# Performance work log

Measured on AMD Instinct MI355X. Metric: run time of the kernel, lower is better.

Reference implementation:

```python
import jax, jax.numpy as jnp
import numpy as np

B, CH, S = 1024, 60, 288
F1, D, F2, NCLS, KL = 8, 2, 16, 4, 64
BN_EPS = 1e-3
PD_EPS = 1e-6  # torch.nn.PairwiseDistance default eps


def _conv(x, w, pad_w=0, groups=1):
    return jax.lax.conv_general_dilated(
        x, w, window_strides=(1, 1), padding=[(0, 0), (pad_w, pad_w)],
        dimension_numbers=("NCHW", "OIHW", "NCHW"), feature_group_count=groups)


def _bn(x, g, b, m, v):
    # eval-mode BatchNorm2d with running stats, eps=0.001
    inv = g / jnp.sqrt(v + BN_EPS)
    return x * inv[None, :, None, None] + (b - m * inv)[None, :, None, None]


def _avgpool_w(x, k):
    s = jax.lax.reduce_window(x, 0.0, jax.lax.add, (1, 1, 1, k), (1, 1, 1, k), "VALID")
    return s / k


def setup_inputs() -> dict:
    key = jax.random.key(0)
    ks = jax.random.split(key, 16)
    x = jax.random.normal(ks[0], (B, 1, CH, S), jnp.float32)
    y = jax.random.randint(ks[1], (B,), 0, NCLS, dtype=jnp.int32)
    conv1_w = jax.random.normal(ks[2], (F1, 1, 1, KL), jnp.float32) * 0.05
    dw = jax.random.normal(ks[3], (F1 * D, 1, CH, 1), jnp.float32) * 0.2
    # Conv2dWithConstraint: torch.renorm(w, p=2, dim=0, maxnorm=1) applied to .data
    norms = jnp.sqrt(jnp.sum(dw * dw, axis=(1, 2, 3), keepdims=True))
    dw_w = dw * jnp.minimum(1.0, 1.0 / jnp.maximum(norms, 1e-7))
    pw_w = jax.random.normal(ks[4], (F2, F1 * D, 1, 1), jnp.float32) * 0.1
    fc_w = jax.random.normal(ks[5], (NCLS, 144), jnp.float32) * 0.05
    fc_b = jnp.zeros((NCLS,), jnp.float32)

    def bnp(k, c):
        k1, k2, k3, k4 = jax.random.split(k, 4)
        g = 1.0 + 0.1 * jax.random.normal(k1, (c,), jnp.float32)
        b = 0.1 * jax.random.normal(k2, (c,), jnp.float32)
        m = 0.1 * jax.random.normal(k3, (c,), jnp.float32)
        v = jax.random.uniform(k4, (c,), jnp.float32, 0.5, 1.5)
        return g, b, m, v

    bn1_g, bn1_b, bn1_m, bn1_v = bnp(ks[6], F1)
    bn2_g, bn2_b, bn2_m, bn2_v = bnp(ks[7], F1 * D)
    bn3_g, bn3_b, bn3_m, bn3_v = bnp(ks[8], F2)
    return dict(x=x, y=y, conv1_w=conv1_w,
                bn1_g=bn1_g, bn1_b=bn1_b, bn1_m=bn1_m, bn1_v=bn1_v,
                dw_w=dw_w, bn2_g=bn2_g, bn2_b=bn2_b, bn2_m=bn2_m, bn2_v=bn2_v,
                pw_w=pw_w, bn3_g=bn3_g, bn3_b=bn3_b, bn3_m=bn3_m, bn3_v=bn3_v,
                fc_w=fc_w, fc_b=fc_b)


def _centroid_loss(feat, y):
    # per-class mean (torch code computes it from detached numpy -> stop_gradient)
    sums = jax.ops.segment_sum(feat, y, num_segments=NCLS)       # [NCLS, 144]
    cnts = jax.ops.segment_sum(jnp.ones((feat.shape[0],), feat.dtype), y, num_segments=NCLS)
    cent = jax.lax.stop_gradient(sums / jnp.maximum(cnts, 1.0)[:, None])
    diff = feat - cent[y] + PD_EPS                                # [B, 144]
    dist = jnp.sqrt(jnp.sum(diff * diff, axis=-1))                # [B]
    return jnp.mean(dist)


def reference(x, y, conv1_w, bn1_g, bn1_b, bn1_m, bn1_v,
              dw_w, bn2_g, bn2_b, bn2_m, bn2_v,
              pw_w, bn3_g, bn3_b, bn3_m, bn3_v, fc_w, fc_b):
    h = _conv(x, conv1_w, pad_w=KL // 2)                 # [B, F1, 60, 289]
    h = _bn(h, bn1_g, bn1_b, bn1_m, bn1_v)
    h = _conv(h, dw_w, pad_w=0, groups=F1)               # [B, F1*D, 1, 289]
    h = _bn(h, bn2_g, bn2_b, bn2_m, bn2_v)
    h = jax.nn.elu(h)
    h = _avgpool_w(h, 4)                                 # width 72 (dropout = eval no-op)
    h = _conv(h, pw_w)                                   # [B, F2, 1, 72]
    h = _bn(h, bn3_g, bn3_b, bn3_m, bn3_v)
    h = jax.nn.elu(h)
    h = _avgpool_w(h, 8)                                 # width 9
    feat = h.reshape(h.shape[0], -1)                     # [B, 144]
    cl = _centroid_loss(feat, y)
    probs = jax.nn.softmax(feat @ fc_w.T + fc_b, axis=1)
    return probs, cl
```

## Files before the change

### kernel.cpp

```cpp
#include <hip/hip_runtime.h>
#include <math.h>

#define NB   1024
#define CH   60
#define SW   288
#define F1C  8
#define FD   16
#define F2C  16
#define KLEN 64
#define NCLS 4
#define PWID 72
#define NV   9
#define FEAT 144
#define NTHR 320
#define ACH  30

#define XR_STRIDE 356
#define PH_STRIDE 76
#define W1_STRIDE 68

__device__ __forceinline__ float elu1(float v) {
    return v > 0.f ? v : __expf(v) - 1.f;
}

__device__ __forceinline__ unsigned short f2bf(float f) {
    unsigned int u = __float_as_uint(f);
    u = (u + 0x7fffu + ((u >> 16) & 1u)) >> 16;
    return (unsigned short)u;
}

__global__ __launch_bounds__(256, 8) void eegnet_chreduce(
    const float* __restrict__ x, const float* __restrict__ dw_w,
    unsigned short* __restrict__ xr,
    float* __restrict__ zero_ws,
    float* __restrict__ cl)
{
    __shared__ float s_part[2][FD][65];
    const int tid = threadIdx.x;
    if (blockIdx.x == 0) {
        for (int i = tid; i < 580; i += 256) zero_ws[i] = 0.f;
        if (tid == 0) cl[0] = 0.f;
    }
    const int wv   = tid >> 6;
    const int lane = tid & 63;
    const int h  = __builtin_amdgcn_readfirstlane(wv & 1);
    const int es = wv >> 1;
    const int e  = blockIdx.x * 2 + es;
    const int wflat = e * 64 + lane;
    const int b = wflat / SW;
    const int w = wflat - b * SW;

    const float* xp = x + (size_t)b * (CH * SW) + (size_t)(h * ACH) * SW + w;
    float v[ACH];
    #pragma unroll
    for (int j = 0; j < ACH; ++j) v[j] = xp[j * SW];

    float acc[FD];
    #pragma unroll
    for (int f = 0; f < FD; ++f) acc[f] = 0.f;
    #pragma unroll
    for (int j = 0; j < ACH; ++j) {
        const float xv = v[j];
        #pragma unroll
        for (int f = 0; f < FD; ++f)
            acc[f] = fmaf(dw_w[f * CH + h * ACH + j], xv, acc[f]);
    }

    if (h == 1) {
        #pragma unroll
        for (int f = 0; f < FD; ++f) s_part[es][f][lane] = acc[f];
    }
    __syncthreads();
    if (h == 0) {
        const size_t base = (size_t)b * (FD * SW) + w;
        #pragma unroll
        for (int f = 0; f < FD; ++f)
            xr[base + f * SW] = f2bf(acc[f] + s_part[es][f][lane]);
    }
}

__global__ __launch_bounds__(NTHR, 4) void eegnet_head(
    const unsigned int* __restrict__ xr, const int* __restrict__ y,
    const float* __restrict__ conv1_w,
    const float* __restrict__ bn1_g, const float* __restrict__ bn1_b,
    const float* __restrict__ bn1_m, const float* __restrict__ bn1_v,
    const float* __restrict__ dw_w,
    const float* __restrict__ bn2_g, const float* __restrict__ bn2_b,
    const float* __restrict__ bn2_m, const float* __restrict__ bn2_v,
    const float* __restrict__ pw_w,
    const float* __restrict__ bn3_g, const float* __restrict__ bn3_b,
    const float* __restrict__ bn3_m, const float* __restrict__ bn3_v,
    const float* __restrict__ fc_w, const float* __restrict__ fc_b,
    float* __restrict__ probs_out, float* __restrict__ feat_out,
    float* __restrict__ sums_out, int* __restrict__ cnt_out)
{
    __shared__ __align__(16) float s_xr[FD * XR_STRIDE];
    __shared__ __align__(16) float s_w1[F1C * W1_STRIDE];
    __shared__ __align__(16) float s_ph[FD * PH_STRIDE];
    __shared__ float s_pwT[FD * F2C];
    __shared__ float s_feat[FEAT];
    __shared__ float s_A[FD], s_Cb[FD], s_a3[F2C], s_c3[F2C];

    const int tid = threadIdx.x;
    const int b = blockIdx.x;

    if (tid == 0) atomicAdd(&cnt_out[y[b]], 1);
    for (int i = tid; i < F1C * KLEN; i += NTHR)
        s_w1[(i >> 6) * W1_STRIDE + (i & 63)] = conv1_w[i];
    for (int i = tid; i < F2C * FD; i += NTHR)
        s_pwT[(i & 15) * F2C + (i >> 4)] = pw_w[i];
    for (int i = tid; i < FD * 68; i += NTHR) {
        int f = i / 68, p = i % 68;
        int wp = (p < 32) ? p : (288 + p);
        s_xr[f * XR_STRIDE + wp] = 0.f;
    }
    {
        const uint4* xrb = (const uint4*)(xr + (size_t)b * (FD * 144));
        for (int i = tid; i < 576; i += NTHR) {
            const int f = i / 36;
            const int k = i - f * 36;
            const uint4 v = xrb[i];
            float* dst = &s_xr[f * XR_STRIDE + 32 + 8 * k];
            float4 lo, hi;
            lo.x = __uint_as_float(v.x << 16); lo.y = __uint_as_float(v.x & 0xffff0000u);
            lo.z = __uint_as_float(v.y << 16); lo.w = __uint_as_float(v.y & 0xffff0000u);
            hi.x = __uint_as_float(v.z << 16); hi.y = __uint_as_float(v.z & 0xffff0000u);
            hi.z = __uint_as_float(v.w << 16); hi.w = __uint_as_float(v.w & 0xffff0000u);
            *(float4*)dst = lo;
            *(float4*)(dst + 4) = hi;
        }
    }
    if (tid < FD) {
        const int f = tid, f1 = f >> 1;
        const float inv1 = bn1_g[f1] / sqrtf(bn1_v[f1] + 1e-3f);
        const float c1 = bn1_b[f1] - bn1_m[f1] * inv1;
        const float inv2 = bn2_g[f] / sqrtf(bn2_v[f] + 1e-3f);
        const float c2 = bn2_b[f] - bn2_m[f] * inv2;
        float sdw = 0.f;
        for (int ch = 0; ch < CH; ++ch) sdw += dw_w[f * CH + ch];
        s_A[f] = inv2 * inv1;
        s_Cb[f] = inv2 * c1 * sdw + c2;
        const float inv3 = bn3_g[f] / sqrtf(bn3_v[f] + 1e-3f);
        s_a3[f] = inv3;
        s_c3[f] = bn3_b[f] - bn3_m[f] * inv3;
    }
    __syncthreads();

    if (tid < 288) {
        const int f = tid & 15;
        const int q = tid >> 4;
        const float4* xp = (const float4*)&s_xr[f * XR_STRIDE + 16 * q];
        const float4* wp = (const float4*)&s_w1[(f >> 1) * W1_STRIDE];
        float cw[20];
        #pragma unroll
        for (int i = 0; i < 4; ++i) {
            const float4 t = xp[i];
            cw[4*i] = t.x; cw[4*i+1] = t.y; cw[4*i+2] = t.z; cw[4*i+3] = t.w;
        }
        float bb[16];
        #pragma unroll
        for (int j = 0; j < 16; ++j) bb[j] = 0.f;
        #pragma unroll
        for (int m = 0; m < 16; ++m) {
            {
                const float4 t = xp[m + 4];
                const int s = (4 * (m + 4)) % 20;
                cw[s] = t.x; cw[s+1] = t.y; cw[s+2] = t.z; cw[s+3] = t.w;
            }
            const float4 wv = wp[m];
            #pragma unroll
            for (int j = 0; j < 16; ++j) {
                bb[j] = fmaf(wv.x, cw[(4*m + j    ) % 20], bb[j]);
                bb[j] = fmaf(wv.y, cw[(4*m + j + 1) % 20], bb[j]);
                bb[j] = fmaf(wv.z, cw[(4*m + j + 2) % 20], bb[j]);
                bb[j] = fmaf(wv.w, cw[(4*m + j + 3) % 20], bb[j]);
            }
        }
        const float Af = s_A[f], Cf = s_Cb[f];
        float e[16];
        #pragma unroll
        for (int j = 0; j < 16; ++j) e[j] = elu1(fmaf(Af, bb[j], Cf));
        float4 ph;
        ph.x = (e[0]  + e[1]  + e[2]  + e[3])  * 0.25f;
        ph.y = (e[4]  + e[5]  + e[6]  + e[7])  * 0.25f;
        ph.z = (e[8]  + e[9]  + e[10] + e[11]) * 0.25f;
        ph.w = (e[12] + e[13] + e[14] + e[15]) * 0.25f;
        *(float4*)&s_ph[f * PH_STRIDE + 4 * q] = ph;
    }
    __syncthreads();

    if (tid < FEAT) {
        const int f2 = tid / NV;
        const int v = tid - f2 * NV;
        float su[8];
        #pragma unroll
        for (int k = 0; k < 8; ++k) su[k] = 0.f;
        #pragma unroll
        for (int f = 0; f < FD; ++f) {
            const float w = s_pwT[f * F2C + f2];
            const float4 p0 = *(const float4*)&s_ph[f * PH_STRIDE + 8 * v];
            const float4 p1 = *(const float4*)&s_ph[f * PH_STRIDE + 8 * v + 4];
            su[0] = fmaf(w, p0.x, su[0]); su[1] = fmaf(w, p0.y, su[1]);
            su[2] = fmaf(w, p0.z, su[2]); su[3] = fmaf(w, p0.w, su[3]);
            su[4] = fmaf(w, p1.x, su[4]); su[5] = fmaf(w, p1.y, su[5]);
            su[6] = fmaf(w, p1.z, su[6]); su[7] = fmaf(w, p1.w, su[7]);
        }
        const float a3f = s_a3[f2], c3f = s_c3[f2];
        float acc = 0.f;
        #pragma unroll
        for (int k = 0; k < 8; ++k) acc += elu1(fmaf(a3f, su[k], c3f));
        const float ft = acc * 0.125f;
        s_feat[tid] = ft;
        feat_out[(size_t)b * FEAT + tid] = ft;
        atomicAdd(&sums_out[y[b] * FEAT + tid], ft);
    }
    __syncthreads();

    if (tid < 64) {
        float lg0 = 0.f, lg1 = 0.f, lg2 = 0.f, lg3 = 0.f;
        for (int j = tid; j < FEAT; j += 64) {
            const float fv = s_feat[j];
            lg0 = fmaf(fv, fc_w[0 * FEAT + j], lg0);
            lg1 = fmaf(fv, fc_w[1 * FEAT + j], lg1);
            lg2 = fmaf(fv, fc_w[2 * FEAT + j], lg2);
            lg3 = fmaf(fv, fc_w[3 * FEAT + j], lg3);
        }
        #pragma unroll
        for (int off = 32; off > 0; off >>= 1) {
            lg0 += __shfl_down(lg0, off, 64);
            lg1 += __shfl_down(lg1, off, 64);
            lg2 += __shfl_down(lg2, off, 64);
            lg3 += __shfl_down(lg3, off, 64);
        }
        if (tid == 0) {
            lg0 += fc_b[0]; lg1 += fc_b[1]; lg2 += fc_b[2]; lg3 += fc_b[3];
            const float m = fmaxf(fmaxf(lg0, lg1), fmaxf(lg2, lg3));
            const float e0 = __expf(lg0 - m), e1 = __expf(lg1 - m);
            const float e2 = __expf(lg2 - m), e3 = __expf(lg3 - m);
            const float inv = 1.f / (e0 + e1 + e2 + e3);
            float* po = probs_out + (size_t)b * NCLS;
            po[0] = e0 * inv; po[1] = e1 * inv; po[2] = e2 * inv; po[3] = e3 * inv;
        }
    }
}

__global__ __launch_bounds__(64) void eegnet_dist(
    const float* __restrict__ feat, const int* __restrict__ y,
    const float* __restrict__ sums, const int* __restrict__ cnt,
    float* __restrict__ cl_out)
{
    __shared__ float s_cent[NCLS * FEAT];
    const int tid = threadIdx.x;
    for (int i = tid; i < NCLS * FEAT; i += 64)
        s_cent[i] = sums[i] / fmaxf((float)cnt[i / FEAT], 1.0f);
    __syncthreads();

    const int s = blockIdx.x * 64 + tid;
    const float* fp = feat + (size_t)s * FEAT;
    const float* cp = &s_cent[y[s] * FEAT];
    float acc = 0.f;
    #pragma unroll
    for (int j = 0; j < FEAT; j += 4) {
        const float4 fv = *reinterpret_cast<const float4*>(fp + j);
        float d;
        d = fv.x - cp[j + 0] + 1e-6f; acc = fmaf(d, d, acc);
        d = fv.y - cp[j + 1] + 1e-6f; acc = fmaf(d, d, acc);
        d = fv.z - cp[j + 2] + 1e-6f; acc = fmaf(d, d, acc);
        d = fv.w - cp[j + 3] + 1e-6f; acc = fmaf(d, d, acc);
    }
    float dist = sqrtf(acc);
    #pragma unroll
    for (int off = 32; off > 0; off >>= 1) dist += __shfl_down(dist, off, 64);
    if (tid == 0) atomicAdd(cl_out, dist * (1.0f / 1024.0f));
}

extern "C" void kernel_launch(void* const* d_in, const int* in_sizes, int n_in,
                              void* d_out, int out_size, void* d_ws, size_t ws_size,
                              hipStream_t stream) {
    const float* x       = (const float*)d_in[0];
    const int*   y       = (const int*)d_in[1];
    const float* conv1_w = (const float*)d_in[2];
    const float* bn1_g   = (const float*)d_in[3];
    const float* bn1_b   = (const float*)d_in[4];
    const float* bn1_m   = (const float*)d_in[5];
    const float* bn1_v   = (const float*)d_in[6];
    const float* dw_w    = (const float*)d_in[7];
    const float* bn2_g   = (const float*)d_in[8];
    const float* bn2_b   = (const float*)d_in[9];
    const float* bn2_m   = (const float*)d_in[10];
    const float* bn2_v   = (const float*)d_in[11];
    const float* pw_w    = (const float*)d_in[12];
    const float* bn3_g   = (const float*)d_in[13];
    const float* bn3_b   = (const float*)d_in[14];
    const float* bn3_m   = (const float*)d_in[15];
    const float* bn3_v   = (const float*)d_in[16];
    const float* fc_w    = (const float*)d_in[17];
    const float* fc_b    = (const float*)d_in[18];

    float* out   = (float*)d_out;
    float* probs = out;
    float* cl    = out + 4096;
    float* sums  = (float*)d_ws;
    int*   cnt   = (int*)((char*)d_ws + 2304);
    float* feat  = (float*)((char*)d_ws + 2560);
    unsigned short* xrbuf = (unsigned short*)((char*)d_ws + 2560 + 589824);

    eegnet_chreduce<<<2304, 256, 0, stream>>>(x, dw_w, xrbuf, sums, cl);
    eegnet_head<<<NB, NTHR, 0, stream>>>(
        (const unsigned int*)xrbuf, y, conv1_w, bn1_g, bn1_b, bn1_m, bn1_v,
        dw_w, bn2_g, bn2_b, bn2_m, bn2_v,
        pw_w, bn3_g, bn3_b, bn3_m, bn3_v,
        fc_w, fc_b, probs, feat, sums, cnt);
    eegnet_dist<<<16, 64, 0, stream>>>(feat, y, sums, cnt, cl);
}
```

Before: 51.15 us.

## Split head kernel into grid-wide conv kernel and per-sample pointwise kernel

The per-sample head kernel is split in two. A new conv kernel runs the temporal conv, BN, ELU and pool across a flat grid, with each thread loading its bf16 window straight from global memory instead of staging it in shared memory. A separate pointwise kernel then reads the pooled activations from a new global buffer. The BN fold constants are computed once in the first kernel and stored in the workspace. This removes the shared-memory staging and the 288-of-320 thread imbalance, but adds a kernel launch and an extra global round trip for the pooled activations.

```diff
diff --git a/kernel.cpp b/kernel.cpp
--- a/kernel.cpp
+++ b/kernel.cpp
@@ -12,10 +12,8 @@
 #define PWID 72
 #define NV   9
 #define FEAT 144
-#define NTHR 320
 #define ACH  30
 
-#define XR_STRIDE 356
 #define PH_STRIDE 76
 #define W1_STRIDE 68
 
@@ -29,9 +27,29 @@
     return (unsigned short)u;
 }
 
+__device__ __forceinline__ float4 bfq_lo(uint4 v) {
+    float4 r;
+    r.x = __uint_as_float(v.x << 16); r.y = __uint_as_float(v.x & 0xffff0000u);
+    r.z = __uint_as_float(v.y << 16); r.w = __uint_as_float(v.y & 0xffff0000u);
+    return r;
+}
+__device__ __forceinline__ float4 bfq_hi(uint4 v) {
+    float4 r;
+    r.x = __uint_as_float(v.z << 16); r.y = __uint_as_float(v.z & 0xffff0000u);
+    r.z = __uint_as_float(v.w << 16); r.w = __uint_as_float(v.w & 0xffff0000u);
+    return r;
+}
+
 __global__ __launch_bounds__(256, 8) void eegnet_chreduce(
     const float* __restrict__ x, const float* __restrict__ dw_w,
+    const float* __restrict__ bn1_g, const float* __restrict__ bn1_b,
+    const float* __restrict__ bn1_m, const float* __restrict__ bn1_v,
+    const float* __restrict__ bn2_g, const float* __restrict__ bn2_b,
+    const float* __restrict__ bn2_m, const float* __restrict__ bn2_v,
+    const float* __restrict__ bn3_g, const float* __restrict__ bn3_b,
+    const float* __restrict__ bn3_m, const float* __restrict__ bn3_v,
     unsigned short* __restrict__ xr,
+    float* __restrict__ folds,
     float* __restrict__ zero_ws,
     float* __restrict__ cl)
 {
@@ -40,6 +58,20 @@
     if (blockIdx.x == 0) {
         for (int i = tid; i < 580; i += 256) zero_ws[i] = 0.f;
         if (tid == 0) cl[0] = 0.f;
+        if (tid < FD) {
+            const int f = tid, f1 = f >> 1;
+            const float inv1 = bn1_g[f1] / sqrtf(bn1_v[f1] + 1e-3f);
+            const float c1 = bn1_b[f1] - bn1_m[f1] * inv1;
+            const float inv2 = bn2_g[f] / sqrtf(bn2_v[f] + 1e-3f);
+            const float c2 = bn2_b[f] - bn2_m[f] * inv2;
+            float sdw = 0.f;
+            for (int ch = 0; ch < CH; ++ch) sdw += dw_w[f * CH + ch];
+            folds[f]      = inv2 * inv1;
+            folds[16 + f] = inv2 * c1 * sdw + c2;
+            const float inv3 = bn3_g[f] / sqrtf(bn3_v[f] + 1e-3f);
+            folds[32 + f] = inv3;
+            folds[48 + f] = bn3_b[f] - bn3_m[f] * inv3;
+        }
     }
     const int wv   = tid >> 6;
     const int lane = tid & 63;
@@ -79,113 +111,98 @@
     }
 }
 
-__global__ __launch_bounds__(NTHR, 4) void eegnet_head(
-    const unsigned int* __restrict__ xr, const int* __restrict__ y,
+__global__ __launch_bounds__(256, 4) void eegnet_conv(
+    const uint4* __restrict__ xr4,
     const float* __restrict__ conv1_w,
-    const float* __restrict__ bn1_g, const float* __restrict__ bn1_b,
-    const float* __restrict__ bn1_m, const float* __restrict__ bn1_v,
-    const float* __restrict__ dw_w,
-    const float* __restrict__ bn2_g, const float* __restrict__ bn2_b,
-    const float* __restrict__ bn2_m, const float* __restrict__ bn2_v,
-    const float* __restrict__ pw_w,
-    const float* __restrict__ bn3_g, const float* __restrict__ bn3_b,
-    const float* __restrict__ bn3_m, const float* __restrict__ bn3_v,
+    const float* __restrict__ folds,
+    float4* __restrict__ ph4)
+{
+    __shared__ __align__(16) float s_w1[F1C * W1_STRIDE];
+    const int tid = threadIdx.x;
+    for (int i = tid; i < F1C * KLEN; i += 256)
+        s_w1[(i >> 6) * W1_STRIDE + (i & 63)] = conv1_w[i];
+
+    const int gid = blockIdx.x * 256 + tid;
+    const int r = gid / 18;
+    const int q = gid - r * 18;
+    const int f = r & 15;
+
+    const uint4* rowp = xr4 + (size_t)r * 36;
+    const int i0 = 2 * q - 4;
+    uint4 u[10];
+    #pragma unroll
+    for (int j = 0; j < 10; ++j) {
+        const int i = i0 + j;
+        if (i >= 0 && i < 36) u[j] = rowp[i];
+        else { u[j].x = 0; u[j].y = 0; u[j].z = 0; u[j].w = 0; }
+    }
+    const float Af = folds[f], Cf = folds[16 + f];
+    __syncthreads();
+
+    float cw[20];
+    {
+        const float4 t0 = bfq_lo(u[0]), t1 = bfq_hi(u[0]);
+        const float4 t2 = bfq_lo(u[1]), t3 = bfq_hi(u[1]);
+        cw[0]=t0.x; cw[1]=t0.y; cw[2]=t0.z; cw[3]=t0.w;
+        cw[4]=t1.x; cw[5]=t1.y; cw[6]=t1.z; cw[7]=t1.w;
+        cw[8]=t2.x; cw[9]=t2.y; cw[10]=t2.z; cw[11]=t2.w;
+        cw[12]=t3.x; cw[13]=t3.y; cw[14]=t3.z; cw[15]=t3.w;
+    }
+    float bb[16];
+    #pragma unroll
+    for (int j = 0; j < 16; ++j) bb[j] = 0.f;
+    const float4* wp = (const float4*)&s_w1[(f >> 1) * W1_STRIDE];
+    #pragma unroll
+    for (int m = 0; m < 16; ++m) {
+        {
+            const float4 t = (m & 1) ? bfq_hi(u[(m + 4) >> 1])
+                                     : bfq_lo(u[(m + 4) >> 1]);
+            const int s = (4 * (m + 4)) % 20;
+            cw[s] = t.x; cw[s+1] = t.y; cw[s+2] = t.z; cw[s+3] = t.w;
+        }
+        const float4 wv = wp[m];
+        #pragma unroll
+        for (int j = 0; j < 16; ++j) {
+            bb[j] = fmaf(wv.x, cw[(4*m + j    ) % 20], bb[j]);
+            bb[j] = fmaf(wv.y, cw[(4*m + j + 1) % 20], bb[j]);
+            bb[j] = fmaf(wv.z, cw[(4*m + j + 2) % 20], bb[j]);
+            bb[j] = fmaf(wv.w, cw[(4*m + j + 3) % 20], bb[j]);
+        }
+    }
+    float e[16];
+    #pragma unroll
+    for (int j = 0; j < 16; ++j) e[j] = elu1(fmaf(Af, bb[j], Cf));
+    float4 ph;
+    ph.x = (e[0]  + e[1]  + e[2]  + e[3])  * 0.25f;
+    ph.y = (e[4]  + e[5]  + e[6]  + e[7])  * 0.25f;
+    ph.z = (e[8]  + e[9]  + e[10] + e[11]) * 0.25f;
+    ph.w = (e[12] + e[13] + e[14] + e[15]) * 0.25f;
+    ph4[gid] = ph;
+}
+
+__global__ __launch_bounds__(256) void eegnet_pw(
+    const float4* __restrict__ ph4, const int* __restrict__ y,
+    const float* __restrict__ folds, const float* __restrict__ pw_w,
     const float* __restrict__ fc_w, const float* __restrict__ fc_b,
     float* __restrict__ probs_out, float* __restrict__ feat_out,
     float* __restrict__ sums_out, int* __restrict__ cnt_out)
 {
-    __shared__ __align__(16) float s_xr[FD * XR_STRIDE];
-    __shared__ __align__(16) float s_w1[F1C * W1_STRIDE];
     __shared__ __align__(16) float s_ph[FD * PH_STRIDE];
     __shared__ float s_pwT[FD * F2C];
     __shared__ float s_feat[FEAT];
-    __shared__ float s_A[FD], s_Cb[FD], s_a3[F2C], s_c3[F2C];
-
     const int tid = threadIdx.x;
     const int b = blockIdx.x;
 
     if (tid == 0) atomicAdd(&cnt_out[y[b]], 1);
-    for (int i = tid; i < F1C * KLEN; i += NTHR)
-        s_w1[(i >> 6) * W1_STRIDE + (i & 63)] = conv1_w[i];
-    for (int i = tid; i < F2C * FD; i += NTHR)
+    for (int i = tid; i < F2C * FD; i += 256)
         s_pwT[(i & 15) * F2C + (i >> 4)] = pw_w[i];
-    for (int i = tid; i < FD * 68; i += NTHR) {
-        int f = i / 68, p = i % 68;
-        int wp = (p < 32) ? p : (288 + p);
-        s_xr[f * XR_STRIDE + wp] = 0.f;
-    }
     {
-        const uint4* xrb = (const uint4*)(xr + (size_t)b * (FD * 144));
-        for (int i = tid; i < 576; i += NTHR) {
-            const int f = i / 36;
-            const int k = i - f * 36;
-            const uint4 v = xrb[i];
-            float* dst = &s_xr[f * XR_STRIDE + 32 + 8 * k];
-            float4 lo, hi;
-            lo.x = __uint_as_float(v.x << 16); lo.y = __uint_as_float(v.x & 0xffff0000u);
-            lo.z = __uint_as_float(v.y << 16); lo.w = __uint_as_float(v.y & 0xffff0000u);
-            hi.x = __uint_as_float(v.z << 16); hi.y = __uint_as_float(v.z & 0xffff0000u);
-            hi.z = __uint_as_float(v.w << 16); hi.w = __uint_as_float(v.w & 0xffff0000u);
-            *(float4*)dst = lo;
-            *(float4*)(dst + 4) = hi;
-        }
-    }
-    if (tid < FD) {
-        const int f = tid, f1 = f >> 1;
-        const float inv1 = bn1_g[f1] / sqrtf(bn1_v[f1] + 1e-3f);
-        const float c1 = bn1_b[f1] - bn1_m[f1] * inv1;
-        const float inv2 = bn2_g[f] / sqrtf(bn2_v[f] + 1e-3f);
-        const float c2 = bn2_b[f] - bn2_m[f] * inv2;
-        float sdw = 0.f;
-        for (int ch = 0; ch < CH; ++ch) sdw += dw_w[f * CH + ch];
-        s_A[f] = inv2 * inv1;
-        s_Cb[f] = inv2 * c1 * sdw + c2;
-        const float inv3 = bn3_g[f] / sqrtf(bn3_v[f] + 1e-3f);
-        s_a3[f] = inv3;
-        s_c3[f] = bn3_b[f] - bn3_m[f] * inv3;
-    }
-    __syncthreads();
-
-    if (tid < 288) {
-        const int f = tid & 15;
-        const int q = tid >> 4;
-        const float4* xp = (const float4*)&s_xr[f * XR_STRIDE + 16 * q];
-        const float4* wp = (const float4*)&s_w1[(f >> 1) * W1_STRIDE];
-        float cw[20];
-        #pragma unroll
-        for (int i = 0; i < 4; ++i) {
-            const float4 t = xp[i];
-            cw[4*i] = t.x; cw[4*i+1] = t.y; cw[4*i+2] = t.z; cw[4*i+3] = t.w;
-        }
-        float bb[16];
-        #pragma unroll
-        for (int j = 0; j < 16; ++j) bb[j] = 0.f;
-        #pragma unroll
-        for (int m = 0; m < 16; ++m) {
-            {
-                const float4 t = xp[m + 4];
-                const int s = (4 * (m + 4)) % 20;
-                cw[s] = t.x; cw[s+1] = t.y; cw[s+2] = t.z; cw[s+3] = t.w;
-            }
-            const float4 wv = wp[m];
-            #pragma unroll
-            for (int j = 0; j < 16; ++j) {
-                bb[j] = fmaf(wv.x, cw[(4*m + j    ) % 20], bb[j]);
-                bb[j] = fmaf(wv.y, cw[(4*m + j + 1) % 20], bb[j]);
-                bb[j] = fmaf(wv.z, cw[(4*m + j + 2) % 20], bb[j]);
-                bb[j] = fmaf(wv.w, cw[(4*m + j + 3) % 20], bb[j]);
-            }
-        }
-        const float Af = s_A[f], Cf = s_Cb[f];
-        float e[16];
-        #pragma unroll
-        for (int j = 0; j < 16; ++j) e[j] = elu1(fmaf(Af, bb[j], Cf));
-        float4 ph;
-        ph.x = (e[0]  + e[1]  + e[2]  + e[3])  * 0.25f;
-        ph.y = (e[4]  + e[5]  + e[6]  + e[7])  * 0.25f;
-        ph.z = (e[8]  + e[9]  + e[10] + e[11]) * 0.25f;
-        ph.w = (e[12] + e[13] + e[14] + e[15]) * 0.25f;
-        *(float4*)&s_ph[f * PH_STRIDE + 4 * q] = ph;
+        const float4* pb = ph4 + (size_t)b * (FD * 18);
+        for (int i = tid; i < FD * 18; i += 256) {
+            const int f = i / 18;
+            const int k = i - f * 18;
+            *(float4*)&s_ph[f * PH_STRIDE + 4 * k] = pb[i];
+        }
     }
     __syncthreads();
 
@@ -205,7 +222,7 @@
             su[4] = fmaf(w, p1.x, su[4]); su[5] = fmaf(w, p1.y, su[5]);
             su[6] = fmaf(w, p1.z, su[6]); su[7] = fmaf(w, p1.w, su[7]);
         }
-        const float a3f = s_a3[f2], c3f = s_c3[f2];
+        const float a3f = folds[32 + f2], c3f = folds[48 + f2];
         float acc = 0.f;
         #pragma unroll
         for (int k = 0; k < 8; ++k) acc += elu1(fmaf(a3f, su[k], c3f));
@@ -300,16 +317,20 @@
     float* out   = (float*)d_out;
     float* probs = out;
     float* cl    = out + 4096;
-    float* sums  = (float*)d_ws;
-    int*   cnt   = (int*)((char*)d_ws + 2304);
-    float* feat  = (float*)((char*)d_ws + 2560);
-    unsigned short* xrbuf = (unsigned short*)((char*)d_ws + 2560 + 589824);
-
-    eegnet_chreduce<<<2304, 256, 0, stream>>>(x, dw_w, xrbuf, sums, cl);
-    eegnet_head<<<NB, NTHR, 0, stream>>>(
-        (const unsigned int*)xrbuf, y, conv1_w, bn1_g, bn1_b, bn1_m, bn1_v,
-        dw_w, bn2_g, bn2_b, bn2_m, bn2_v,
-        pw_w, bn3_g, bn3_b, bn3_m, bn3_v,
-        fc_w, fc_b, probs, feat, sums, cnt);
+    char*  ws    = (char*)d_ws;
+    float* sums  = (float*)ws;
+    int*   cnt   = (int*)(ws + 2304);
+    float* folds = (float*)(ws + 2432);
+    float* feat  = (float*)(ws + 2816);
+    unsigned short* xrbuf = (unsigned short*)(ws + 2816 + 589824);
+    float4* phbuf = (float4*)(ws + 2816 + 589824 + 9437184);
+
+    eegnet_chreduce<<<2304, 256, 0, stream>>>(
+        x, dw_w, bn1_g, bn1_b, bn1_m, bn1_v, bn2_g, bn2_b, bn2_m, bn2_v,
+        bn3_g, bn3_b, bn3_m, bn3_v, xrbuf, folds, sums, cl);
+    eegnet_conv<<<1152, 256, 0, stream>>>(
+        (const uint4*)xrbuf, conv1_w, folds, phbuf);
+    eegnet_pw<<<NB, 256, 0, stream>>>(
+        phbuf, y, folds, pw_w, fc_w, fc_b, probs, feat, sums, cnt);
     eegnet_dist<<<16, 64, 0, stream>>>(feat, y, sums, cnt, cl);
 }
```

New measurement: 54.09 us. +5.8%, slower.
